# Optimization experiments

Hardware: AMD Instinct MI355X
Metric: run time of the kernel (lower is better)

The kernel has to match this reference:

```python
import jax, jax.numpy as jnp
import numpy as np

EPS_LN = 1e-6
EPS_BN = 1e-5
NUM_HEADS = 8


def _dwconv(img, w, b=None, stride=1):
    # img: (B,C,H,W), w: (C,1,k,k) depthwise
    out = jax.lax.conv_general_dilated(
        img, w, (stride, stride), 'SAME',
        feature_group_count=img.shape[1],
        dimension_numbers=('NCHW', 'OIHW', 'NCHW'))
    if b is not None:
        out = out + b[None, :, None, None]
    return out


def _layernorm(x, g, b):
    m = jnp.mean(x, axis=-1, keepdims=True)
    v = jnp.mean(jnp.square(x - m), axis=-1, keepdims=True)
    return (x - m) * jax.lax.rsqrt(v + EPS_LN) * g + b


def _hardswish(x):
    return x * jnp.clip(x + 3.0, 0.0, 6.0) * (1.0 / 6.0)


def _forward(img, domain_label, pe_dw_w, pe_pw_w, pe_bn_g, pe_bn_b, pe_bn_m, pe_bn_v,
             cpe_w, cpe_b, norm1_g, norm1_b, qkv_w, qkv_b,
             crpe_w3, crpe_b3, crpe_w5, crpe_b5, crpe_w7, crpe_b7,
             dom_w1, dom_b1, dom_w2, dom_b2, proj_w, proj_b,
             norm2_g, norm2_b, fc1_w, fc1_b, fc2_w, fc2_b, d):
    B = img.shape[0]
    # --- DWCPatchEmbed_M: depthwise 3x3 s2 + pointwise 1x1 + domain BN (eval) + hardswish ---
    x = _dwconv(img, pe_dw_w, None, stride=2)                      # (B,Cin,H,W)
    x = jax.lax.conv_general_dilated(x, pe_pw_w, (1, 1), 'SAME',
                                     dimension_numbers=('NCHW', 'OIHW', 'NCHW'))
    g, be, mu, var = pe_bn_g[d], pe_bn_b[d], pe_bn_m[d], pe_bn_v[d]
    scale_bn = g * jax.lax.rsqrt(var + EPS_BN)
    x = (x - mu[None, :, None, None]) * scale_bn[None, :, None, None] + be[None, :, None, None]
    x = _hardswish(x)
    _, C, H, W = x.shape
    N = H * W
    x = x.reshape(B, C, N).transpose(0, 2, 1)                      # (B,N,C) tokens

    # --- ConvPosEnc: depthwise 3x3 on image layout, residual ---
    img2 = x.transpose(0, 2, 1).reshape(B, C, H, W)
    x = x + _dwconv(img2, cpe_w, cpe_b).reshape(B, C, N).transpose(0, 2, 1)

    # --- FactorAtt_ConvRelPosEnc_Sup ---
    cur = _layernorm(x, norm1_g[d], norm1_b[d])
    h = NUM_HEADS
    Ch = C // h
    qkv = cur @ qkv_w + qkv_b                                      # (B,N,3C)
    qkv = qkv.reshape(B, N, 3, h, Ch).transpose(2, 0, 3, 1, 4)     # (3,B,h,N,Ch)
    q, k, v = qkv[0], qkv[1], qkv[2]
    k_sm = jax.nn.softmax(k, axis=2)                               # softmax over tokens
    kv = jnp.einsum('bhnk,bhnv->bhkv', k_sm, v)                    # (B,h,Ch,Ch)
    factor_att = jnp.einsum('bhnk,bhkv->bhnv', q, kv)              # (B,h,N,Ch)

    # conv relative position encoding: windows {3:2heads, 5:3heads, 7:3heads}
    v_img = v.transpose(0, 1, 3, 2).reshape(B, C, H, W)            # (B, h*Ch, H, W)
    s1, s2 = 2 * Ch, 5 * Ch
    cv = jnp.concatenate([
        _dwconv(v_img[:, :s1], crpe_w3, crpe_b3),
        _dwconv(v_img[:, s1:s2], crpe_w5, crpe_b5),
        _dwconv(v_img[:, s2:], crpe_w7, crpe_b7)], axis=1)
    cv = cv.reshape(B, h, Ch, N).transpose(0, 1, 3, 2)             # (B,h,N,Ch)
    crpe = q * cv

    factor_att = (Ch ** -0.5) * factor_att + crpe

    # domain gate: Linear->ReLU->Linear on one-hot, softmax over heads
    da = jax.nn.relu(domain_label @ dom_w1 + dom_b1) @ dom_w2 + dom_b2   # (B,C)
    da = da.reshape(B, h, Ch)[:, :, None, :]                        # (B,h,1,Ch)
    da = jax.nn.softmax(da, axis=1)
    out = da * factor_att                                           # (B,h,N,Ch)
    out = out.transpose(0, 2, 1, 3).reshape(B, N, C)
    out = out @ proj_w + proj_b
    x = x + out

    # --- MLP (ratio 8), domain LayerNorm, residual ---
    cur = _layernorm(x, norm2_g[d], norm2_b[d])
    cur = jax.nn.gelu(cur @ fc1_w + fc1_b, approximate=False) @ fc2_w + fc2_b
    x = x + cur
    return x


def setup_inputs() -> dict:
    key = jax.random.key(0)
    ks = jax.random.split(key, 16)
    B, Cin, Hin, Win = 8, 64, 128, 128
    C, h, D = 128, NUM_HEADS, 4
    Ch = C // h
    hid_dom = C // 2
    hid_mlp = 8 * C
    f = jnp.float32

    def n(k, shape, s=0.02):
        return (s * jax.random.normal(k, shape)).astype(f)

    img = jax.random.normal(ks[0], (B, Cin, Hin, Win), dtype=f)
    domain_label = jax.nn.one_hot(jnp.zeros((B,), jnp.int32), D, dtype=f)
    return dict(
        img=img, domain_label=domain_label,
        pe_dw_w=n(ks[1], (Cin, 1, 3, 3), 0.1),
        pe_pw_w=n(ks[2], (C, Cin, 1, 1), 0.1),
        pe_bn_g=jnp.ones((D, C), f), pe_bn_b=jnp.zeros((D, C), f),
        pe_bn_m=n(ks[3], (D, C), 0.1),
        pe_bn_v=jnp.ones((D, C), f),
        cpe_w=n(ks[4], (C, 1, 3, 3), 0.1), cpe_b=jnp.zeros((C,), f),
        norm1_g=jnp.ones((D, C), f), norm1_b=jnp.zeros((D, C), f),
        qkv_w=n(ks[5], (C, 3 * C)), qkv_b=jnp.zeros((3 * C,), f),
        crpe_w3=n(ks[6], (2 * Ch, 1, 3, 3), 0.1), crpe_b3=jnp.zeros((2 * Ch,), f),
        crpe_w5=n(ks[7], (3 * Ch, 1, 5, 5), 0.1), crpe_b5=jnp.zeros((3 * Ch,), f),
        crpe_w7=n(ks[8], (3 * Ch, 1, 7, 7), 0.1), crpe_b7=jnp.zeros((3 * Ch,), f),
        dom_w1=n(ks[9], (D, hid_dom)), dom_b1=jnp.zeros((hid_dom,), f),
        dom_w2=n(ks[10], (hid_dom, C)), dom_b2=jnp.zeros((C,), f),
        proj_w=n(ks[11], (C, C)), proj_b=jnp.zeros((C,), f),
        norm2_g=jnp.ones((D, C), f), norm2_b=jnp.zeros((D, C), f),
        fc1_w=n(ks[12], (C, hid_mlp)), fc1_b=jnp.zeros((hid_mlp,), f),
        fc2_w=n(ks[13], (hid_mlp, C)), fc2_b=jnp.zeros((C,), f),
        d=0,
    )


def reference(img, domain_label, pe_dw_w, pe_pw_w, pe_bn_g, pe_bn_b, pe_bn_m, pe_bn_v,
              cpe_w, cpe_b, norm1_g, norm1_b, qkv_w, qkv_b,
              crpe_w3, crpe_b3, crpe_w5, crpe_b5, crpe_w7, crpe_b7,
              dom_w1, dom_b1, dom_w2, dom_b2, proj_w, proj_b,
              norm2_g, norm2_b, fc1_w, fc1_b, fc2_w, fc2_b, d):
    return _forward(img, domain_label, pe_dw_w, pe_pw_w, pe_bn_g, pe_bn_b, pe_bn_m, pe_bn_v,
                    cpe_w, cpe_b, norm1_g, norm1_b, qkv_w, qkv_b,
                    crpe_w3, crpe_b3, crpe_w5, crpe_b5, crpe_w7, crpe_b7,
                    dom_w1, dom_b1, dom_w2, dom_b2, proj_w, proj_b,
                    norm2_g, norm2_b, fc1_w, fc1_b, fc2_w, fc2_b, d)
```

## Files before the change

kernel.cpp:

```cpp
#include <hip/hip_runtime.h>
#include <math.h>

#define EPS_LN 1e-6f
#define EPS_BN 1e-5f

typedef __attribute__((ext_vector_type(8))) short bf16x8;
typedef __attribute__((ext_vector_type(4))) float f32x4;

__device__ __forceinline__ float wave_reduce_sum(float v) {
    #pragma unroll
    for (int m = 32; m >= 1; m >>= 1) v += __shfl_xor(v, m, 64);
    return v;
}
__device__ __forceinline__ float wave_reduce_max(float v) {
    #pragma unroll
    for (int m = 32; m >= 1; m >>= 1) v = fmaxf(v, __shfl_xor(v, m, 64));
    return v;
}
__device__ __forceinline__ short f2bf(float f) {
    union { float f; unsigned u; } v; v.f = f;
    unsigned r = v.u + 0x7fff + ((v.u >> 16) & 1);
    return (short)(r >> 16);
}
__device__ __forceinline__ unsigned pack2bf(float a, float b) {
    return (unsigned)(unsigned short)f2bf(a) | ((unsigned)(unsigned short)f2bf(b) << 16);
}
__device__ __forceinline__ float gelu_f(float x) {
    float x2 = x * x;
    float u = x * (-1.595769122f - 0.071354816f * x2) * 1.0f;
    float e = __expf(u);
    return x * __builtin_amdgcn_rcpf(1.f + e);
}

__global__ __launch_bounds__(256) void pe_kernel(
    const float* __restrict__ img, const float* __restrict__ dww,
    const float* __restrict__ pww, const float* __restrict__ bn_g,
    const float* __restrict__ bn_b, const float* __restrict__ bn_m,
    const float* __restrict__ bn_v, const int* __restrict__ dptr,
    float* __restrict__ t1) {
    __shared__ float dw[64 * 68];
    __shared__ float wsm[64 * 132];
    int bx = blockIdx.x;
    int b = bx >> 6, y = bx & 63;
    int tid = threadIdx.x;
    int d = *dptr;

    for (int idx = tid; idx < 8192; idx += 256) {
        int co = idx >> 6, ci = idx & 63;
        wsm[ci * 132 + co] = pww[idx];
    }

    for (int it = 0; it < 4; ++it) {
        int task = tid + it * 256;
        int ci = task >> 4, xx0 = (task & 15) * 4;
        const float* ip = img + (size_t)(b * 64 + ci) * 16384;
        const float* wd = dww + ci * 9;
        float a0 = 0.f, a1 = 0.f, a2 = 0.f, a3 = 0.f;
        #pragma unroll
        for (int r = 0; r < 3; ++r) {
            int iy = 2 * y + r;
            if (iy >= 128) continue;
            const float* rp = ip + iy * 128 + 2 * xx0;
            float u[9];
            *(f32x4*)&u[0] = *(const f32x4*)rp;
            *(f32x4*)&u[4] = *(const f32x4*)(rp + 4);
            u[8] = (xx0 < 60) ? rp[8] : 0.f;
            #pragma unroll
            for (int s = 0; s < 3; ++s) {
                float w = wd[r * 3 + s];
                a0 += u[s] * w;
                a1 += u[2 + s] * w;
                a2 += u[4 + s] * w;
                a3 += u[6 + s] * w;
            }
        }
        f32x4 st = {a0, a1, a2, a3};
        *(f32x4*)&dw[ci * 68 + xx0] = st;
    }
    __syncthreads();

    int xg = tid & 15, cog = tid >> 4;
    int xx0 = xg * 4, co0 = cog * 8;
    f32x4 acc[8];
    f32x4 zr = {0.f, 0.f, 0.f, 0.f};
    #pragma unroll
    for (int i = 0; i < 8; ++i) acc[i] = zr;
    for (int ci = 0; ci < 64; ++ci) {
        f32x4 dv = *(const f32x4*)&dw[ci * 68 + xx0];
        f32x4 w0 = *(const f32x4*)&wsm[ci * 132 + co0];
        f32x4 w1 = *(const f32x4*)&wsm[ci * 132 + co0 + 4];
        acc[0] += dv * w0.x; acc[1] += dv * w0.y;
        acc[2] += dv * w0.z; acc[3] += dv * w0.w;
        acc[4] += dv * w1.x; acc[5] += dv * w1.y;
        acc[6] += dv * w1.z; acc[7] += dv * w1.w;
    }
    #pragma unroll
    for (int i = 0; i < 8; ++i) {
        int co = co0 + i;
        float sc = bn_g[d * 128 + co] * rsqrtf(bn_v[d * 128 + co] + EPS_BN);
        float mu = bn_m[d * 128 + co], be = bn_b[d * 128 + co];
        f32x4 v = (acc[i] - mu) * sc + be;
        f32x4 r;
        r.x = v.x * fminf(fmaxf(v.x + 3.f, 0.f), 6.f) * (1.f / 6.f);
        r.y = v.y * fminf(fmaxf(v.y + 3.f, 0.f), 6.f) * (1.f / 6.f);
        r.z = v.z * fminf(fmaxf(v.z + 3.f, 0.f), 6.f) * (1.f / 6.f);
        r.w = v.w * fminf(fmaxf(v.w + 3.f, 0.f), 6.f) * (1.f / 6.f);
        *(f32x4*)&t1[(size_t)(b * 128 + co) * 4096 + y * 64 + xx0] = r;
    }
}

__global__ __launch_bounds__(256) void cpe_kernel(
    const float* __restrict__ t1, const float* __restrict__ cw,
    const float* __restrict__ cb, float* __restrict__ xout) {
    int bx = blockIdx.x;
    int cq = bx & 3, y = (bx >> 2) & 63, b = bx >> 8;
    int c0 = cq * 32;
    __shared__ float s[3 * 32 * 65];
    int tid = threadIdx.x;
    for (int idx = tid; idx < 3 * 32 * 64; idx += 256) {
        int xx = idx & 63;
        int cl = (idx >> 6) & 31;
        int dy = idx >> 11;
        int yy = y + dy - 1;
        float v = 0.f;
        if (yy >= 0 && yy < 64)
            v = t1[(size_t)(b * 128 + c0 + cl) * 4096 + yy * 64 + xx];
        s[(dy * 32 + cl) * 65 + xx] = v;
    }
    __syncthreads();
    for (int idx = tid; idx < 32 * 64; idx += 256) {
        int cl = idx & 31;
        int xx = idx >> 5;
        int c = c0 + cl;
        float center = s[(32 + cl) * 65 + xx];
        float acc = cb[c];
        #pragma unroll
        for (int dy = 0; dy < 3; ++dy) {
            #pragma unroll
            for (int dx = 0; dx < 3; ++dx) {
                int sx = xx + dx - 1;
                if (sx < 0 || sx >= 64) continue;
                acc += s[(dy * 32 + cl) * 65 + sx] * cw[c * 9 + dy * 3 + dx];
            }
        }
        xout[(size_t)(b * 4096 + y * 64 + xx) * 128 + c] = center + acc;
    }
}

__global__ __launch_bounds__(256) void prep_kernel(
    const float* __restrict__ qkv_w, const float* __restrict__ n1_g,
    const float* __restrict__ n1_b, const float* __restrict__ qkv_b,
    const float* __restrict__ pw, const float* __restrict__ f1w,
    const float* __restrict__ n2_g, const float* __restrict__ n2_b,
    const float* __restrict__ f1b, const float* __restrict__ f2w,
    const float* __restrict__ dl, const float* __restrict__ dw1,
    const float* __restrict__ db1, const float* __restrict__ dw2,
    const float* __restrict__ db2, const int* __restrict__ dptr,
    short* __restrict__ qkvp, short* __restrict__ pwp,
    short* __restrict__ w1p, short* __restrict__ w2p,
    float* __restrict__ qbp, float* __restrict__ f1bp,
    float* __restrict__ da) {
    __shared__ float sh[1536];
    int bb = blockIdx.x;
    int tid = threadIdx.x;
    int d = *dptr;
    if (bb < 24) {
        int idx = bb * 256 + tid;
        int l = idx & 63, kk = (idx >> 6) & 3, n = idx >> 8;
        int k0 = kk * 32 + (l >> 4) * 8;
        int c = n * 16 + (l & 15);
        bf16x8 v;
        #pragma unroll
        for (int j = 0; j < 8; ++j)
            v[j] = f2bf(n1_g[d * 128 + k0 + j] * qkv_w[(size_t)(k0 + j) * 384 + c]);
        *(bf16x8*)&qkvp[(size_t)idx * 8] = v;
    } else if (bb < 32) {
        int idx = (bb - 24) * 256 + tid;
        int l = idx & 63, kk = (idx >> 6) & 3, n = idx >> 8;
        int k0 = kk * 32 + (l >> 4) * 8;
        int c = n * 16 + (l & 15);
        bf16x8 v;
        #pragma unroll
        for (int j = 0; j < 8; ++j) v[j] = f2bf(pw[(size_t)(k0 + j) * 128 + c]);
        *(bf16x8*)&pwp[(size_t)idx * 8] = v;
    } else if (bb < 96) {
        int idx = (bb - 32) * 256 + tid;
        int l = idx & 63, kk = (idx >> 6) & 3, n = idx >> 8;
        int k0 = kk * 32 + (l >> 4) * 8;
        int c = n * 16 + (l & 15);
        bf16x8 v;
        #pragma unroll
        for (int j = 0; j < 8; ++j)
            v[j] = f2bf(n2_g[d * 128 + k0 + j] * f1w[(size_t)(k0 + j) * 1024 + c]);
        *(bf16x8*)&w1p[(size_t)idx * 8] = v;
    } else if (bb < 160) {
        int idx = (bb - 96) * 256 + tid;
        int l = idx & 63, kk = (idx >> 6) & 31, n = idx >> 11;
        int k0 = kk * 32 + (l >> 4) * 8;
        int c = n * 16 + (l & 15);
        bf16x8 v;
        #pragma unroll
        for (int j = 0; j < 8; ++j) v[j] = f2bf(f2w[(size_t)(k0 + j) * 128 + c]);
        *(bf16x8*)&w2p[(size_t)idx * 8] = v;
    } else if (bb < 162) {
        int j = (bb - 160) * 256 + tid;
        if (j < 384) {
            float s = qkv_b[j];
            for (int k = 0; k < 128; ++k)
                s += n1_b[d * 128 + k] * qkv_w[(size_t)k * 384 + j];
            qbp[j] = s;
        }
    } else if (bb < 166) {
        int j = (bb - 162) * 256 + tid;
        float s = f1b[j];
        for (int k = 0; k < 128; ++k)
            s += n2_b[d * 128 + k] * f1w[(size_t)k * 1024 + j];
        f1bp[j] = s;
    } else {
        float* hid = sh;
        float* raw = sh + 512;
        for (int idx = tid; idx < 512; idx += 256) {
            int b = idx >> 6, jj = idx & 63;
            float a = db1[jj];
            #pragma unroll
            for (int dd = 0; dd < 4; ++dd)
                a += dl[b * 4 + dd] * dw1[dd * 64 + jj];
            hid[idx] = fmaxf(a, 0.f);
        }
        __syncthreads();
        for (int idx = tid; idx < 1024; idx += 256) {
            int b = idx >> 7, c = idx & 127;
            float a = db2[c];
            for (int jj = 0; jj < 64; ++jj)
                a += hid[b * 64 + jj] * dw2[jj * 128 + c];
            raw[idx] = a;
        }
        __syncthreads();
        if (tid < 128) {
            int b = tid >> 4, ch = tid & 15;
            float mx = -1e30f;
            #pragma unroll
            for (int hh = 0; hh < 8; ++hh)
                mx = fmaxf(mx, raw[b * 128 + hh * 16 + ch]);
            float e[8];
            float s = 0.f;
            #pragma unroll
            for (int hh = 0; hh < 8; ++hh) {
                e[hh] = expf(raw[b * 128 + hh * 16 + ch] - mx);
                s += e[hh];
            }
            float inv = 1.f / s;
            #pragma unroll
            for (int hh = 0; hh < 8; ++hh)
                da[b * 128 + hh * 16 + ch] = e[hh] * inv;
        }
    }
}

__global__ __launch_bounds__(512, 4) void qkv_mfma_kernel(
    const float* __restrict__ x, const short* __restrict__ wp,
    const float* __restrict__ biasp, float* __restrict__ q_img,
    float* __restrict__ k_img, float* __restrict__ v_img) {
    int tb = blockIdx.x * 32;
    int tid = threadIdx.x;
    int lane = tid & 63, wv = tid >> 6;
    int tt = wv & 1, g = wv >> 1;
    int lhi = lane >> 4, llo = lane & 15;
    int b = tb >> 12, n0 = tb & 4095;

    bf16x8 afr[4];
    {
        f32x4 v0[4], v1[4];
        float sum = 0.f;
        #pragma unroll
        for (int kk = 0; kk < 4; ++kk) {
            const float* p = x + (size_t)(tb + tt * 16 + llo) * 128 + kk * 32 + lhi * 8;
            v0[kk] = *(const f32x4*)p;
            v1[kk] = *(const f32x4*)(p + 4);
            sum += v0[kk].x + v0[kk].y + v0[kk].z + v0[kk].w
                 + v1[kk].x + v1[kk].y + v1[kk].z + v1[kk].w;
        }
        sum += __shfl_xor(sum, 16, 64);
        sum += __shfl_xor(sum, 32, 64);
        float mean = sum * (1.f / 128.f);
        float vs = 0.f;
        #pragma unroll
        for (int kk = 0; kk < 4; ++kk) {
            f32x4 a = v0[kk], c = v1[kk];
            float d0 = a.x - mean, d1 = a.y - mean, d2 = a.z - mean, d3 = a.w - mean;
            float d4 = c.x - mean, d5 = c.y - mean, d6 = c.z - mean, d7 = c.w - mean;
            vs += d0*d0 + d1*d1 + d2*d2 + d3*d3 + d4*d4 + d5*d5 + d6*d6 + d7*d7;
        }
        vs += __shfl_xor(vs, 16, 64);
        vs += __shfl_xor(vs, 32, 64);
        float rs = rsqrtf(vs * (1.f / 128.f) + EPS_LN);
        #pragma unroll
        for (int kk = 0; kk < 4; ++kk) {
            bf16x8 o;
            o[0] = f2bf((v0[kk].x - mean) * rs);
            o[1] = f2bf((v0[kk].y - mean) * rs);
            o[2] = f2bf((v0[kk].z - mean) * rs);
            o[3] = f2bf((v0[kk].w - mean) * rs);
            o[4] = f2bf((v1[kk].x - mean) * rs);
            o[5] = f2bf((v1[kk].y - mean) * rs);
            o[6] = f2bf((v1[kk].z - mean) * rs);
            o[7] = f2bf((v1[kk].w - mean) * rs);
            afr[kk] = o;
        }
    }

    f32x4 acc[6];
    f32x4 zr = {0.f, 0.f, 0.f, 0.f};
    #pragma unroll
    for (int i = 0; i < 6; ++i) acc[i] = zr;

    #pragma unroll
    for (int i = 0; i < 6; ++i) {
        int nb = g * 6 + i;
        #pragma unroll
        for (int kk = 0; kk < 4; ++kk) {
            bf16x8 wf = *(const bf16x8*)&wp[((size_t)(nb * 4 + kk) * 64 + lane) * 8];
            acc[i] = __builtin_amdgcn_mfma_f32_16x16x32_bf16(wf, afr[kk], acc[i], 0, 0, 0);
        }
    }

    #pragma unroll
    for (int i = 0; i < 6; ++i) {
        int j0 = (g * 6 + i) * 16;
        f32x4 bv = *(const f32x4*)(biasp + j0 + lhi * 4);
        float* dst = (j0 < 128) ? q_img : ((j0 < 256) ? k_img : v_img);
        int c0 = (j0 & 127) + lhi * 4;
        f32x4 r = acc[i] + bv;
        float* p = dst + (size_t)(b * 128 + c0) * 4096 + n0 + tt * 16 + llo;
        p[0]        = r.x;
        p[4096]     = r.y;
        p[2 * 4096] = r.z;
        p[3 * 4096] = r.w;
    }
}

__global__ __launch_bounds__(256) void softmax_kernel(float* __restrict__ k_img) {
    __shared__ float red[4];
    float* p = k_img + (size_t)blockIdx.x * 4096;
    int tid = threadIdx.x;
    float v[16];
    float mx = -1e30f;
    #pragma unroll
    for (int i = 0; i < 16; ++i) {
        v[i] = p[tid + i * 256];
        mx = fmaxf(mx, v[i]);
    }
    mx = wave_reduce_max(mx);
    int wid = tid >> 6, lane = tid & 63;
    if (lane == 0) red[wid] = mx;
    __syncthreads();
    mx = fmaxf(fmaxf(red[0], red[1]), fmaxf(red[2], red[3]));
    __syncthreads();
    float sum = 0.f;
    #pragma unroll
    for (int i = 0; i < 16; ++i) {
        v[i] = expf(v[i] - mx);
        sum += v[i];
    }
    sum = wave_reduce_sum(sum);
    if (lane == 0) red[wid] = sum;
    __syncthreads();
    float inv = 1.f / (red[0] + red[1] + red[2] + red[3]);
    #pragma unroll
    for (int i = 0; i < 16; ++i)
        p[tid + i * 256] = v[i] * inv;
}

__global__ __launch_bounds__(256) void kv_part_kernel(
    const float* __restrict__ k_img, const float* __restrict__ v_img,
    float* __restrict__ kvp) {
    __shared__ float ks[16 * 132], vs[16 * 132];
    int bc = blockIdx.x;
    int bh = bc >> 3, chunk = bc & 7;
    int b = bh >> 3, h = bh & 7;
    int tid = threadIdx.x;
    int ck = tid >> 4, cv = tid & 15;
    float acc = 0.f;
    const float* kp = k_img + (size_t)(b * 128 + h * 16) * 4096;
    const float* vp = v_img + (size_t)(b * 128 + h * 16) * 4096;
    int nb0 = chunk * 512;
    for (int nb = nb0; nb < nb0 + 512; nb += 128) {
        for (int idx = tid; idx < 2048; idx += 256) {
            int r = idx >> 7, col = idx & 127;
            ks[r * 132 + col] = kp[(size_t)r * 4096 + nb + col];
            vs[r * 132 + col] = vp[(size_t)r * 4096 + nb + col];
        }
        __syncthreads();
        for (int kk = 0; kk < 128; ++kk)
            acc += ks[ck * 132 + kk] * vs[cv * 132 + kk];
        __syncthreads();
    }
    kvp[(size_t)(chunk * 64 + bh) * 256 + ck * 16 + cv] = acc;
}

__global__ __launch_bounds__(256) void fa_kernel(
    const float* __restrict__ q_img, const float* __restrict__ kvp,
    float* __restrict__ fa_img) {
    __shared__ float kvs[256];
    int bid = blockIdx.x;
    int bh = bid >> 4, chunk = bid & 15;
    int b = bh >> 3, h = bh & 7;
    int tid = threadIdx.x;
    {
        float s = 0.f;
        #pragma unroll
        for (int c = 0; c < 8; ++c) s += kvp[(size_t)c * 16384 + bh * 256 + tid];
        kvs[tid] = s;
    }
    __syncthreads();
    int n = chunk * 256 + tid;
    const float* qp = q_img + (size_t)(b * 128 + h * 16) * 4096 + n;
    float qv[16];
    #pragma unroll
    for (int ck = 0; ck < 16; ++ck) qv[ck] = qp[(size_t)ck * 4096];
    float* fp = fa_img + (size_t)(b * 128 + h * 16) * 4096 + n;
    #pragma unroll
    for (int cv = 0; cv < 16; ++cv) {
        float s = 0.f;
        #pragma unroll
        for (int ck = 0; ck < 16; ++ck) s += qv[ck] * kvs[ck * 16 + cv];
        fp[(size_t)cv * 4096] = s;
    }
}

template<int KC>
__device__ __forceinline__ void conv4(const float* __restrict__ s,
                                      const float* __restrict__ wsm,
                                      int y, int xx0, float* a4) {
    const int OFF = KC / 2;
    #pragma unroll
    for (int dy = 0; dy < KC; ++dy) {
        int sy = y + dy - OFF;
        if (sy < 0 || sy >= 64) continue;
        const float* r = s + sy * 72;
        float u[12];
        *(f32x4*)&u[0] = *(const f32x4*)&r[xx0];
        *(f32x4*)&u[4] = *(const f32x4*)&r[xx0 + 4];
        *(f32x4*)&u[8] = *(const f32x4*)&r[xx0 + 8];
        #pragma unroll
        for (int dx = 0; dx < KC; ++dx) {
            float w = wsm[dy * KC + dx];
            const int base = dx - OFF + 4;
            a4[0] += u[base + 0] * w;
            a4[1] += u[base + 1] * w;
            a4[2] += u[base + 2] * w;
            a4[3] += u[base + 3] * w;
        }
    }
}

__global__ __launch_bounds__(256) void att_kernel(
    const float* __restrict__ q_img, const float* __restrict__ v_img,
    const float* __restrict__ fa_img, const float* __restrict__ da,
    const float* __restrict__ w3, const float* __restrict__ b3,
    const float* __restrict__ w5, const float* __restrict__ b5,
    const float* __restrict__ w7, const float* __restrict__ b7,
    float* __restrict__ att) {
    __shared__ float s[64 * 72];
    __shared__ float wsm[49];
    int o = ((blockIdx.x & 7) << 7) | (blockIdx.x >> 3);
    int b = o >> 7, c = o & 127;
    int tid = threadIdx.x;
    const float* vp = v_img + (size_t)(b * 128 + c) * 4096;
    for (int idx = tid; idx < 4096; idx += 256) {
        int row = idx >> 6, xx = idx & 63;
        s[row * 72 + xx + 4] = vp[idx];
    }
    for (int idx = tid; idx < 512; idx += 256) {
        int row = idx >> 3, j = idx & 7;
        s[row * 72 + (j < 4 ? j : 64 + j)] = 0.f;
    }
    int kc; const float* wp; float bias;
    if (c < 32)      { kc = 3; wp = w3 + c * 9;         bias = b3[c]; }
    else if (c < 80) { kc = 5; wp = w5 + (c - 32) * 25; bias = b5[c - 32]; }
    else             { kc = 7; wp = w7 + (c - 80) * 49; bias = b7[c - 80]; }
    if (tid < kc * kc) wsm[tid] = wp[tid];
    float dac = da[b * 128 + c];
    size_t rowbase = (size_t)(b * 128 + c) * 4096;
    __syncthreads();
    for (int it = 0; it < 4; ++it) {
        int task = tid + it * 256;
        int y = task >> 4, xx0 = (task & 15) * 4;
        float a4[4] = {bias, bias, bias, bias};
        if (kc == 3)      conv4<3>(s, wsm, y, xx0, a4);
        else if (kc == 5) conv4<5>(s, wsm, y, xx0, a4);
        else              conv4<7>(s, wsm, y, xx0, a4);
        size_t base = rowbase + y * 64 + xx0;
        f32x4 fav = *(const f32x4*)&fa_img[base];
        f32x4 qv  = *(const f32x4*)&q_img[base];
        f32x4 cv4 = {a4[0], a4[1], a4[2], a4[3]};
        f32x4 r = (fav * 0.25f + qv * cv4) * dac;
        *(f32x4*)&att[base] = r;
    }
}

__global__ __launch_bounds__(256, 2) void proj_mfma_kernel(
    const float* __restrict__ att, const short* __restrict__ wp,
    const float* __restrict__ bias, const float* __restrict__ xres,
    float* __restrict__ out) {
    __shared__ float As[128 * 33];
    int tb = blockIdx.x * 32;
    int tid = threadIdx.x;
    int lane = tid & 63, wv = tid >> 6;
    int lhi = lane >> 4, llo = lane & 15;
    int b = tb >> 12, n0 = tb & 4095;

    for (int idx = tid; idx < 4096; idx += 256) {
        int c = idx >> 5, t = idx & 31;
        As[c * 33 + t] = att[(size_t)(b * 128 + c) * 4096 + n0 + t];
    }
    __syncthreads();

    bf16x8 afr[2][4];
    #pragma unroll
    for (int tt = 0; tt < 2; ++tt) {
        #pragma unroll
        for (int kk = 0; kk < 4; ++kk) {
            int c0 = kk * 32 + lhi * 8;
            int t = tt * 16 + llo;
            bf16x8 v;
            #pragma unroll
            for (int j = 0; j < 8; ++j) v[j] = f2bf(As[(c0 + j) * 33 + t]);
            afr[tt][kk] = v;
        }
    }

    f32x4 acc[2][2];
    f32x4 zr = {0.f, 0.f, 0.f, 0.f};
    #pragma unroll
    for (int i = 0; i < 2; ++i) { acc[i][0] = zr; acc[i][1] = zr; }

    #pragma unroll
    for (int i = 0; i < 2; ++i) {
        int nb = wv * 2 + i;
        #pragma unroll
        for (int kk = 0; kk < 4; ++kk) {
            bf16x8 wf = *(const bf16x8*)&wp[((size_t)(nb * 4 + kk) * 64 + lane) * 8];
            acc[i][0] = __builtin_amdgcn_mfma_f32_16x16x32_bf16(wf, afr[0][kk], acc[i][0], 0, 0, 0);
            acc[i][1] = __builtin_amdgcn_mfma_f32_16x16x32_bf16(wf, afr[1][kk], acc[i][1], 0, 0, 0);
        }
    }

    #pragma unroll
    for (int i = 0; i < 2; ++i) {
        int j0 = (wv * 2 + i) * 16;
        f32x4 bv = *(const f32x4*)(bias + j0 + lhi * 4);
        #pragma unroll
        for (int tt = 0; tt < 2; ++tt) {
            size_t o = (size_t)(tb + tt * 16 + llo) * 128 + j0 + lhi * 4;
            f32x4 xr = *(const f32x4*)(xres + o);
            *(f32x4*)(out + o) = xr + acc[i][tt] + bv;
        }
    }
}

__global__ __launch_bounds__(512, 3) void mlp_mfma_kernel(
    const short* __restrict__ w1p, const float* __restrict__ b1p,
    const short* __restrict__ w2p, const float* __restrict__ b2,
    float* io) {
    __shared__ short hs[32768];
    int tb = blockIdx.x * 32;
    int tid = threadIdx.x;
    int lane = tid & 63, wv = tid >> 6;
    int lhi = lane >> 4, llo = lane & 15;

    bf16x8 afr[2][4];
    #pragma unroll
    for (int tt = 0; tt < 2; ++tt) {
        f32x4 v0[4], v1[4];
        float sum = 0.f;
        #pragma unroll
        for (int kk = 0; kk < 4; ++kk) {
            const float* p = io + (size_t)(tb + tt * 16 + llo) * 128 + kk * 32 + lhi * 8;
            v0[kk] = *(const f32x4*)p;
            v1[kk] = *(const f32x4*)(p + 4);
            sum += v0[kk].x + v0[kk].y + v0[kk].z + v0[kk].w
                 + v1[kk].x + v1[kk].y + v1[kk].z + v1[kk].w;
        }
        sum += __shfl_xor(sum, 16, 64);
        sum += __shfl_xor(sum, 32, 64);
        float mean = sum * (1.f / 128.f);
        float vs = 0.f;
        #pragma unroll
        for (int kk = 0; kk < 4; ++kk) {
            f32x4 a = v0[kk], c = v1[kk];
            float d0 = a.x - mean, d1 = a.y - mean, d2 = a.z - mean, d3 = a.w - mean;
            float d4 = c.x - mean, d5 = c.y - mean, d6 = c.z - mean, d7 = c.w - mean;
            vs += d0*d0 + d1*d1 + d2*d2 + d3*d3 + d4*d4 + d5*d5 + d6*d6 + d7*d7;
        }
        vs += __shfl_xor(vs, 16, 64);
        vs += __shfl_xor(vs, 32, 64);
        float rs = rsqrtf(vs * (1.f / 128.f) + EPS_LN);
        #pragma unroll
        for (int kk = 0; kk < 4; ++kk) {
            bf16x8 o;
            o[0] = f2bf((v0[kk].x - mean) * rs);
            o[1] = f2bf((v0[kk].y - mean) * rs);
            o[2] = f2bf((v0[kk].z - mean) * rs);
            o[3] = f2bf((v0[kk].w - mean) * rs);
            o[4] = f2bf((v1[kk].x - mean) * rs);
            o[5] = f2bf((v1[kk].y - mean) * rs);
            o[6] = f2bf((v1[kk].z - mean) * rs);
            o[7] = f2bf((v1[kk].w - mean) * rs);
            afr[tt][kk] = o;
        }
    }

    f32x4 acc[2][8];
    f32x4 zr = {0.f, 0.f, 0.f, 0.f};
    #pragma unroll
    for (int tt = 0; tt < 2; ++tt)
        #pragma unroll
        for (int nl = 0; nl < 8; ++nl) acc[tt][nl] = zr;

    const short* wbase = w1p + (size_t)(wv * 8) * 4 * 64 * 8;
    #pragma unroll
    for (int nl = 0; nl < 8; ++nl) {
        #pragma unroll
        for (int kk = 0; kk < 4; ++kk) {
            bf16x8 bf = *(const bf16x8*)(wbase + ((size_t)(nl * 4 + kk) * 64 + lane) * 8);
            acc[0][nl] = __builtin_amdgcn_mfma_f32_16x16x32_bf16(bf, afr[0][kk], acc[0][nl], 0, 0, 0);
            acc[1][nl] = __builtin_amdgcn_mfma_f32_16x16x32_bf16(bf, afr[1][kk], acc[1][nl], 0, 0, 0);
        }
    }

    #pragma unroll
    for (int nl = 0; nl < 8; ++nl) {
        int hn = wv * 8 + nl;
        int hc0 = hn * 16 + lhi * 4;
        f32x4 bv = *(const f32x4*)(b1p + hc0);
        int kk2 = hn >> 1;
        int lp = llo + 16 * ((hn & 1) * 2 + (lhi >> 1));
        #pragma unroll
        for (int tt = 0; tt < 2; ++tt) {
            f32x4 a = acc[tt][nl] + bv;
            uint2 wv2;
            wv2.x = pack2bf(gelu_f(a.x), gelu_f(a.y));
            wv2.y = pack2bf(gelu_f(a.z), gelu_f(a.w));
            *(uint2*)((char*)hs + ((size_t)(tt * 32 + kk2) * 64 + lp) * 16 + (lhi & 1) * 8) = wv2;
        }
    }
    __syncthreads();

    f32x4 acc2[2];
    acc2[0] = zr; acc2[1] = zr;

    const short* w2base = w2p + (size_t)wv * 32 * 64 * 8;
    #pragma unroll 4
    for (int kk2 = 0; kk2 < 32; ++kk2) {
        bf16x8 h0 = *(const bf16x8*)&hs[((size_t)(0 * 32 + kk2) * 64 + lane) * 8];
        bf16x8 h1 = *(const bf16x8*)&hs[((size_t)(1 * 32 + kk2) * 64 + lane) * 8];
        bf16x8 w0 = *(const bf16x8*)(w2base + ((size_t)kk2 * 64 + lane) * 8);
        acc2[0] = __builtin_amdgcn_mfma_f32_16x16x32_bf16(w0, h0, acc2[0], 0, 0, 0);
        acc2[1] = __builtin_amdgcn_mfma_f32_16x16x32_bf16(w0, h1, acc2[1], 0, 0, 0);
    }

    int c0 = wv * 16 + lhi * 4;
    f32x4 bv = *(const f32x4*)(b2 + c0);
    #pragma unroll
    for (int tt2 = 0; tt2 < 2; ++tt2) {
        float* op = io + (size_t)(tb + tt2 * 16 + llo) * 128 + c0;
        f32x4 r = *(f32x4*)op;
        r = r + acc2[tt2] + bv;
        *(f32x4*)op = r;
    }
}

extern "C" void kernel_launch(void* const* d_in, const int* in_sizes, int n_in,
                              void* d_out, int out_size, void* d_ws, size_t ws_size,
                              hipStream_t stream) {
    const float* img   = (const float*)d_in[0];
    const float* dl    = (const float*)d_in[1];
    const float* pe_dw = (const float*)d_in[2];
    const float* pe_pw = (const float*)d_in[3];
    const float* bn_g  = (const float*)d_in[4];
    const float* bn_b  = (const float*)d_in[5];
    const float* bn_m  = (const float*)d_in[6];
    const float* bn_v  = (const float*)d_in[7];
    const float* cpe_w = (const float*)d_in[8];
    const float* cpe_b = (const float*)d_in[9];
    const float* n1_g  = (const float*)d_in[10];
    const float* n1_b  = (const float*)d_in[11];
    const float* qkv_w = (const float*)d_in[12];
    const float* qkv_b = (const float*)d_in[13];
    const float* w3    = (const float*)d_in[14];
    const float* b3    = (const float*)d_in[15];
    const float* w5    = (const float*)d_in[16];
    const float* b5    = (const float*)d_in[17];
    const float* w7    = (const float*)d_in[18];
    const float* b7    = (const float*)d_in[19];
    const float* dw1   = (const float*)d_in[20];
    const float* db1   = (const float*)d_in[21];
    const float* dw2   = (const float*)d_in[22];
    const float* db2   = (const float*)d_in[23];
    const float* pw    = (const float*)d_in[24];
    const float* pb    = (const float*)d_in[25];
    const float* n2_g  = (const float*)d_in[26];
    const float* n2_b  = (const float*)d_in[27];
    const float* f1w   = (const float*)d_in[28];
    const float* f1b   = (const float*)d_in[29];
    const float* f2w   = (const float*)d_in[30];
    const float* f2b   = (const float*)d_in[31];
    const int*   dptr  = (const int*)d_in[32];
    float* out = (float*)d_out;

    char* ws = (char*)d_ws;
    const size_t SZ = (size_t)8 * 128 * 4096 * 4;
    float* t1    = (float*)(ws);
    float* x     = (float*)(ws + SZ);
    float* q_img = (float*)(ws + 2 * SZ);
    float* k_img = (float*)(ws + 3 * SZ);
    float* v_img = (float*)(ws + 4 * SZ);
    float* da    = (float*)(ws + 5 * SZ + 0x10000);
    short* qkvp  = (short*)(ws + 5 * SZ + 0x20000);
    short* pwp   = (short*)(ws + 5 * SZ + 0x40000);
    float* qbp   = (float*)(ws + 5 * SZ + 0x48000);
    float* f1bp  = (float*)(ws + 5 * SZ + 0x4A000);
    float* kvp   = (float*)(ws + 5 * SZ + 0x50000);
    short* w1p   = (short*)(ws + 5 * SZ + 0xD0000);
    short* w2p   = (short*)(ws + 5 * SZ + 0x110000);
    float* fa_img = t1;

    prep_kernel<<<167, 256, 0, stream>>>(qkv_w, n1_g, n1_b, qkv_b, pw, f1w,
                                         n2_g, n2_b, f1b, f2w, dl, dw1, db1,
                                         dw2, db2, dptr, qkvp, pwp, w1p, w2p,
                                         qbp, f1bp, da);
    pe_kernel<<<512, 256, 0, stream>>>(img, pe_dw, pe_pw, bn_g, bn_b, bn_m, bn_v, dptr, t1);
    cpe_kernel<<<2048, 256, 0, stream>>>(t1, cpe_w, cpe_b, x);
    qkv_mfma_kernel<<<1024, 512, 0, stream>>>(x, qkvp, qbp, q_img, k_img, v_img);
    softmax_kernel<<<1024, 256, 0, stream>>>(k_img);
    kv_part_kernel<<<512, 256, 0, stream>>>(k_img, v_img, kvp);
    fa_kernel<<<1024, 256, 0, stream>>>(q_img, kvp, fa_img);
    att_kernel<<<1024, 256, 0, stream>>>(q_img, v_img, fa_img, da, w3, b3, w5, b5, w7, b7, k_img);
    proj_mfma_kernel<<<1024, 256, 0, stream>>>(k_img, pwp, pb, x, out);
    mlp_mfma_kernel<<<1024, 512, 0, stream>>>(w1p, f1bp, w2p, f2b, out);
}
```

Baseline: 337.9 us.

## Split MLP hidden dim into two passes to halve LDS and raise occupancy

```diff
diff --git a/kernel.cpp b/kernel.cpp
--- a/kernel.cpp
+++ b/kernel.cpp
@@ -27,7 +27,7 @@
 }
 __device__ __forceinline__ float gelu_f(float x) {
     float x2 = x * x;
-    float u = x * (-1.595769122f - 0.071354816f * x2) * 1.0f;
+    float u = x * (-1.595769122f - 0.071354816f * x2);
     float e = __expf(u);
     return x * __builtin_amdgcn_rcpf(1.f + e);
 }
@@ -559,19 +559,19 @@
     }
 }
 
-__global__ __launch_bounds__(512, 3) void mlp_mfma_kernel(
+__global__ __launch_bounds__(512, 6) void mlp_mfma_kernel(
     const short* __restrict__ w1p, const float* __restrict__ b1p,
     const short* __restrict__ w2p, const float* __restrict__ b2,
     float* io) {
-    __shared__ short hs[32768];
+    __shared__ short afs[2 * 4 * 64 * 8];
+    __shared__ short hs[2 * 16 * 64 * 8];
     int tb = blockIdx.x * 32;
     int tid = threadIdx.x;
     int lane = tid & 63, wv = tid >> 6;
     int lhi = lane >> 4, llo = lane & 15;
 
-    bf16x8 afr[2][4];
-    #pragma unroll
-    for (int tt = 0; tt < 2; ++tt) {
+    if (wv < 2) {
+        int tt = wv;
         f32x4 v0[4], v1[4];
         float sum = 0.f;
         #pragma unroll
@@ -607,57 +607,69 @@
             o[5] = f2bf((v1[kk].y - mean) * rs);
             o[6] = f2bf((v1[kk].z - mean) * rs);
             o[7] = f2bf((v1[kk].w - mean) * rs);
-            afr[tt][kk] = o;
-        }
-    }
-
-    f32x4 acc[2][8];
+            *(bf16x8*)&afs[((size_t)(tt * 4 + kk) * 64 + lane) * 8] = o;
+        }
+    }
+    __syncthreads();
+
+    bf16x8 afr[2][4];
+    #pragma unroll
+    for (int tt = 0; tt < 2; ++tt)
+        #pragma unroll
+        for (int kk = 0; kk < 4; ++kk)
+            afr[tt][kk] = *(const bf16x8*)&afs[((size_t)(tt * 4 + kk) * 64 + lane) * 8];
+
     f32x4 zr = {0.f, 0.f, 0.f, 0.f};
-    #pragma unroll
-    for (int tt = 0; tt < 2; ++tt)
-        #pragma unroll
-        for (int nl = 0; nl < 8; ++nl) acc[tt][nl] = zr;
-
-    const short* wbase = w1p + (size_t)(wv * 8) * 4 * 64 * 8;
-    #pragma unroll
-    for (int nl = 0; nl < 8; ++nl) {
-        #pragma unroll
-        for (int kk = 0; kk < 4; ++kk) {
-            bf16x8 bf = *(const bf16x8*)(wbase + ((size_t)(nl * 4 + kk) * 64 + lane) * 8);
-            acc[0][nl] = __builtin_amdgcn_mfma_f32_16x16x32_bf16(bf, afr[0][kk], acc[0][nl], 0, 0, 0);
-            acc[1][nl] = __builtin_amdgcn_mfma_f32_16x16x32_bf16(bf, afr[1][kk], acc[1][nl], 0, 0, 0);
-        }
-    }
-
-    #pragma unroll
-    for (int nl = 0; nl < 8; ++nl) {
-        int hn = wv * 8 + nl;
-        int hc0 = hn * 16 + lhi * 4;
-        f32x4 bv = *(const f32x4*)(b1p + hc0);
-        int kk2 = hn >> 1;
-        int lp = llo + 16 * ((hn & 1) * 2 + (lhi >> 1));
-        #pragma unroll
-        for (int tt = 0; tt < 2; ++tt) {
-            f32x4 a = acc[tt][nl] + bv;
-            uint2 wv2;
-            wv2.x = pack2bf(gelu_f(a.x), gelu_f(a.y));
-            wv2.y = pack2bf(gelu_f(a.z), gelu_f(a.w));
-            *(uint2*)((char*)hs + ((size_t)(tt * 32 + kk2) * 64 + lp) * 16 + (lhi & 1) * 8) = wv2;
-        }
-    }
-    __syncthreads();
-
     f32x4 acc2[2];
     acc2[0] = zr; acc2[1] = zr;
 
-    const short* w2base = w2p + (size_t)wv * 32 * 64 * 8;
-    #pragma unroll 4
-    for (int kk2 = 0; kk2 < 32; ++kk2) {
-        bf16x8 h0 = *(const bf16x8*)&hs[((size_t)(0 * 32 + kk2) * 64 + lane) * 8];
-        bf16x8 h1 = *(const bf16x8*)&hs[((size_t)(1 * 32 + kk2) * 64 + lane) * 8];
-        bf16x8 w0 = *(const bf16x8*)(w2base + ((size_t)kk2 * 64 + lane) * 8);
-        acc2[0] = __builtin_amdgcn_mfma_f32_16x16x32_bf16(w0, h0, acc2[0], 0, 0, 0);
-        acc2[1] = __builtin_amdgcn_mfma_f32_16x16x32_bf16(w0, h1, acc2[1], 0, 0, 0);
+    #pragma unroll
+    for (int p = 0; p < 2; ++p) {
+        f32x4 acc[2][4];
+        #pragma unroll
+        for (int tt = 0; tt < 2; ++tt)
+            #pragma unroll
+            for (int nl = 0; nl < 4; ++nl) acc[tt][nl] = zr;
+
+        const short* wbase = w1p + (size_t)(p * 32 + wv * 4) * 4 * 64 * 8;
+        #pragma unroll
+        for (int nl = 0; nl < 4; ++nl) {
+            #pragma unroll
+            for (int kk = 0; kk < 4; ++kk) {
+                bf16x8 bf = *(const bf16x8*)(wbase + ((size_t)(nl * 4 + kk) * 64 + lane) * 8);
+                acc[0][nl] = __builtin_amdgcn_mfma_f32_16x16x32_bf16(bf, afr[0][kk], acc[0][nl], 0, 0, 0);
+                acc[1][nl] = __builtin_amdgcn_mfma_f32_16x16x32_bf16(bf, afr[1][kk], acc[1][nl], 0, 0, 0);
+            }
+        }
+
+        #pragma unroll
+        for (int nl = 0; nl < 4; ++nl) {
+            int hn = p * 32 + wv * 4 + nl;
+            int kk2l = wv * 2 + (nl >> 1);
+            int hc0 = hn * 16 + lhi * 4;
+            f32x4 bv = *(const f32x4*)(b1p + hc0);
+            int lp = llo + 16 * ((hn & 1) * 2 + (lhi >> 1));
+            #pragma unroll
+            for (int tt = 0; tt < 2; ++tt) {
+                f32x4 a = acc[tt][nl] + bv;
+                uint2 wv2;
+                wv2.x = pack2bf(gelu_f(a.x), gelu_f(a.y));
+                wv2.y = pack2bf(gelu_f(a.z), gelu_f(a.w));
+                *(uint2*)((char*)hs + ((size_t)(tt * 16 + kk2l) * 64 + lp) * 16 + (lhi & 1) * 8) = wv2;
+            }
+        }
+        __syncthreads();
+
+        const short* w2base = w2p + (size_t)(wv * 32 + p * 16) * 64 * 8;
+        #pragma unroll 4
+        for (int kk2l = 0; kk2l < 16; ++kk2l) {
+            bf16x8 h0 = *(const bf16x8*)&hs[((size_t)(0 * 16 + kk2l) * 64 + lane) * 8];
+            bf16x8 h1 = *(const bf16x8*)&hs[((size_t)(1 * 16 + kk2l) * 64 + lane) * 8];
+            bf16x8 w0 = *(const bf16x8*)(w2base + ((size_t)kk2l * 64 + lane) * 8);
+            acc2[0] = __builtin_amdgcn_mfma_f32_16x16x32_bf16(w0, h0, acc2[0], 0, 0, 0);
+            acc2[1] = __builtin_amdgcn_mfma_f32_16x16x32_bf16(w0, h1, acc2[1], 0, 0, 0);
+        }
+        if (p == 0) __syncthreads();
     }
 
     int c0 = wv * 16 + lhi * 4;
```

New measurement: 367.7 us. +8.8%, slower.
